# Kernel optimization log

Measured on AMD Instinct MI355X. Metric: run time of the kernel, lower is better.

Reference implementation:

```python
import jax, jax.numpy as jnp
import numpy as np

B, S, D = 4, 8192, 768
H, HD = 12, 64
CS, NL = 512, 32


def setup_inputs() -> dict:
    key = jax.random.key(0)
    ks = jax.random.split(key, 9)
    sc = 0.02
    return {
        "x": jax.random.normal(ks[0], (B, S, D), jnp.float32),
        "q_w": jax.random.normal(ks[1], (D, D), jnp.float32) * sc,
        "q_b": jax.random.normal(ks[2], (D,), jnp.float32) * sc,
        "k_w": jax.random.normal(ks[3], (D, D), jnp.float32) * sc,
        "k_b": jax.random.normal(ks[4], (D,), jnp.float32) * sc,
        "v_w": jax.random.normal(ks[5], (D, D), jnp.float32) * sc,
        "v_b": jax.random.normal(ks[6], (D,), jnp.float32) * sc,
        "o_w": jax.random.normal(ks[7], (D, D), jnp.float32) * sc,
        "o_b": jax.random.normal(ks[8], (D,), jnp.float32) * sc,
    }


def reference(x, q_w, q_b, k_w, k_b, v_w, v_b, o_w, o_b):
    # x: (B, S, D); S divisible by CS and NL -> no padding / trimming needed.
    scale = HD ** -0.5
    n_chunks = S // CS
    seg = S // NL
    # Global landmarks: mean-pool NL evenly spaced segments. (B, NL, D)
    landmarks = x.reshape(B, NL, seg, D).mean(axis=2)
    # Q only over local tokens (torch Linear: x @ W^T + b)
    q = (x @ q_w.T + q_b).reshape(B, n_chunks, CS, H, HD)
    x_chunks = x.reshape(B, n_chunks, CS, D)
    # Prepend landmarks to every chunk's KV context: ctx = NL + CS
    lm = jnp.broadcast_to(landmarks[:, None], (B, n_chunks, NL, D))
    kv_ctx = jnp.concatenate([lm, x_chunks], axis=2)  # (B, n_chunks, ctx, D)
    ctx = NL + CS
    k = (kv_ctx @ k_w.T + k_b).reshape(B, n_chunks, ctx, H, HD)
    v = (kv_ctx @ v_w.T + v_b).reshape(B, n_chunks, ctx, H, HD)
    scores = jnp.einsum("bnqhd,bnkhd->bnhqk", q, k) * scale
    attn = jax.nn.softmax(scores, axis=-1)  # dropout=0 (eval)
    out = jnp.einsum("bnhqk,bnkhd->bnqhd", attn, v).reshape(B, S, D)
    return out @ o_w.T + o_b
```

## Files before the change

kernel.cpp:

```cpp
#include <hip/hip_runtime.h>


typedef unsigned short u16;
typedef __attribute__((ext_vector_type(8))) short short8;
typedef __attribute__((ext_vector_type(4))) float f32x4;

__device__ __forceinline__ u16 f2bf(float f) {
    unsigned u = __float_as_uint(f);
    u += 0x7fffu + ((u >> 16) & 1u);
    return (u16)(u >> 16);
}

#define MFMA_BF16(A, B, C) __builtin_amdgcn_mfma_f32_16x16x32_bf16((A), (B), (C), 0, 0, 0)

__device__ __forceinline__ void gload16(const u16* g, const short* l) {
    __builtin_amdgcn_global_load_lds(
        (__attribute__((address_space(1))) void*)g,
        (__attribute__((address_space(3))) void*)l, 16, 0, 0);
}

__global__ __launch_bounds__(256) void k_cvtx(const float* __restrict__ x,
                                              u16* __restrict__ xa,
                                              float* __restrict__ part) {
    const int g = blockIdx.x;
    const int t = threadIdx.x;
    const float* base = x + (size_t)g * 64 * 768;
    u16* ob = xa + (size_t)g * 64 * 768;
    float s0 = 0.f, s1 = 0.f, s2 = 0.f;
    for (int r = 0; r < 64; ++r) {
        const size_t off = (size_t)r * 768;
        const float v0 = base[off + t], v1 = base[off + t + 256], v2 = base[off + t + 512];
        s0 += v0; s1 += v1; s2 += v2;
        ob[off + t] = f2bf(v0); ob[off + t + 256] = f2bf(v1); ob[off + t + 512] = f2bf(v2);
    }
    float* p = part + (size_t)g * 768;
    p[t] = s0; p[t + 256] = s1; p[t + 512] = s2;
}

__global__ void k_lmred(const float* __restrict__ part, u16* __restrict__ xa_lm) {
    const int bl = blockIdx.x;
    const int t = threadIdx.x;
    const float* p = part + (size_t)bl * 4 * 768;
    const float inv = 1.f / 256.f;
    for (int c = t; c < 768; c += 256) {
        const float s = p[c] + p[768 + c] + p[1536 + c] + p[2304 + c];
        xa_lm[(size_t)bl * 768 + c] = f2bf(s * inv);
    }
}

__global__ void k_cvtw(const float* __restrict__ qw, const float* __restrict__ kw,
                       const float* __restrict__ vw, const float* __restrict__ ow,
                       const float* __restrict__ qb, const float* __restrict__ kb,
                       const float* __restrict__ vb,
                       u16* __restrict__ wcat, u16* __restrict__ owb,
                       float* __restrict__ bcat) {
    const int yy = blockIdx.y;
    const int i = blockIdx.x * 256 + threadIdx.x;
    if (yy == 4) {
        if (i < 768)       bcat[i] = qb[i];
        else if (i < 1536) bcat[i] = kb[i - 768];
        else if (i < 2304) bcat[i] = vb[i - 1536];
        return;
    }
    const float* src = (yy == 0) ? qw : (yy == 1) ? kw : (yy == 2) ? vw : ow;
    u16* dst = (yy == 3) ? owb : wcat + (size_t)yy * 589824;
    const float4 v = ((const float4*)src)[i];
    ushort4 o;
    o.x = f2bf(v.x); o.y = f2bf(v.y); o.z = f2bf(v.z); o.w = f2bf(v.w);
    ((ushort4*)dst)[i] = o;
}

template <int MODE>
__global__ __launch_bounds__(512, 4) void k_gemm(
    const u16* __restrict__ A, const u16* __restrict__ Bw, const float* __restrict__ bias,
    u16* __restrict__ qx, u16* __restrict__ ktok, u16* __restrict__ vt,
    u16* __restrict__ klm, u16* __restrict__ vlmt, float* __restrict__ outf)
{
    __shared__ short lA[2][4096];
    __shared__ short lB[2][8192];
    const int t = threadIdx.x;
    const int wid = t >> 6, lane = t & 63, lr = lane & 15, lg = lane >> 4;
    const int wm = wid >> 2, wn = wid & 3;

    const int gx = gridDim.x;
    const int nwg = gx * gridDim.y;
    const int orig = blockIdx.x + gx * blockIdx.y;
    const int qq = nwg >> 3, rr = nwg & 7, xcd = orig & 7, ii = orig >> 3;
    const int wg = (xcd < rr ? xcd * (qq + 1) : rr * (qq + 1) + (xcd - rr) * qq) + ii;
    const int m0 = (wg / gx) * 128, n0 = (wg % gx) * 256;

    const int rA = t >> 2,        cA = ((t & 3) ^ ((rA >> 1) & 3)) * 8;
    const int rB0 = t >> 2,       cB0 = cA;
    const int uB1 = 512 + t;
    const int rB1 = uB1 >> 2,     cB1 = (((uB1) & 3) ^ ((rB1 >> 1) & 3)) * 8;
    const u16* pa0 = A  + (size_t)(m0 + rA) * 768 + cA;
    const u16* pb0 = Bw + (size_t)(n0 + rB0) * 768 + cB0;
    const u16* pb1 = Bw + (size_t)(n0 + rB1) * 768 + cB1;
    const int sa = (lg ^ ((lr >> 1) & 3)) * 8;

#define STG(S, T) {                                            \
    gload16(pa0 + (T) * 32, &lA[S][wid * 512]);                \
    gload16(pb0 + (T) * 32, &lB[S][wid * 512]);                \
    gload16(pb1 + (T) * 32, &lB[S][4096 + wid * 512]); }

    f32x4 acc[4][4] = {};
    STG(0, 0); STG(1, 1);

#pragma unroll
    for (int T = 0; T < 24; ++T) {
        const int s = T & 1;
        if (T < 23) asm volatile("s_waitcnt vmcnt(3)" ::: "memory");
        else        asm volatile("s_waitcnt vmcnt(0)" ::: "memory");
        __builtin_amdgcn_s_barrier();
        __builtin_amdgcn_sched_barrier(0);
        short8 aq[4], bq[4];
#pragma unroll
        for (int mf = 0; mf < 4; ++mf)
            aq[mf] = *(const short8*)&lA[s][(wm * 64 + mf * 16 + lr) * 32 + sa];
#pragma unroll
        for (int nf = 0; nf < 4; ++nf)
            bq[nf] = *(const short8*)&lB[s][(wn * 64 + nf * 16 + lr) * 32 + sa];
        asm volatile("s_waitcnt lgkmcnt(0)" ::: "memory");
        __builtin_amdgcn_sched_barrier(0);
        __builtin_amdgcn_s_barrier();
        if (T + 2 < 24) STG(s, T + 2);
        __builtin_amdgcn_s_setprio(1);
#pragma unroll
        for (int mf = 0; mf < 4; ++mf)
#pragma unroll
            for (int nf = 0; nf < 4; ++nf)
                acc[mf][nf] = MFMA_BF16(aq[mf], bq[nf], acc[mf][nf]);
        __builtin_amdgcn_s_setprio(0);
    }
#undef STG

    if (MODE == 0) {
        const int region = n0 / 768;
        if (region == 2) {
#pragma unroll
            for (int nf = 0; nf < 4; ++nf) {
                const int gn = n0 + wn * 64 + nf * 16 + lr;
                const float bv = bias[gn];
                const int nn = gn - 1536;
                const int h = nn >> 6, d = nn & 63;
#pragma unroll
                for (int mf = 0; mf < 4; ++mf) {
                    const int gmb = m0 + wm * 64 + mf * 16 + lg * 4;
                    ushort4 w;
                    w.x = f2bf(acc[mf][nf][0] + bv);
                    w.y = f2bf(acc[mf][nf][1] + bv);
                    w.z = f2bf(acc[mf][nf][2] + bv);
                    w.w = f2bf(acc[mf][nf][3] + bv);
                    if (gmb < 32768) {
                        const int b = gmb >> 13, ss = gmb & 8191;
                        *(ushort4*)(vt + ((size_t)(b * 12 + h) * 64 + d) * 8192 + ss) = w;
                    } else {
                        const int ii2 = gmb - 32768;
                        const int bb = ii2 >> 5, lmr = ii2 & 31;
                        *(ushort4*)(vlmt + ((size_t)(bb * 12 + h) * 64 + d) * 32 + lmr) = w;
                    }
                }
            }
        } else {
            u16* dst = (region == 0) ? qx : ktok;
#pragma unroll
            for (int nf = 0; nf < 4; ++nf) {
                const int gn = n0 + wn * 64 + nf * 16 + lr;
                const int nn = gn - region * 768;
                const int h = nn >> 6, d = nn & 63;
                const float bv = bias[gn];
#pragma unroll
                for (int mf = 0; mf < 4; ++mf) {
                    const int gmb = m0 + wm * 64 + mf * 16 + lg * 4;
#pragma unroll
                    for (int r = 0; r < 4; ++r) {
                        const int gm = gmb + r;
                        const u16 val = f2bf(acc[mf][nf][r] + bv);
                        if (gm < 32768) {
                            const int b = gm >> 13, ss = gm & 8191;
                            dst[((size_t)(b * 12 + h) * 8192 + ss) * 64 + d] = val;
                        } else if (region == 1) {
                            const int ii2 = gm - 32768;
                            klm[((size_t)((ii2 >> 5) * 12 + h) * 32 + (ii2 & 31)) * 64 + d] = val;
                        }
                    }
                }
            }
        }
    } else {
#pragma unroll
        for (int nf = 0; nf < 4; ++nf) {
            const int gn = n0 + wn * 64 + nf * 16 + lr;
            const float bvv = bias[gn];
#pragma unroll
            for (int mf = 0; mf < 4; ++mf) {
                const int gmb = m0 + wm * 64 + mf * 16 + lg * 4;
#pragma unroll
                for (int r = 0; r < 4; ++r)
                    outf[(size_t)(gmb + r) * 768 + gn] = acc[mf][nf][r] + bvv;
            }
        }
    }
}

__global__ __launch_bounds__(256) void k_attn(
    const u16* __restrict__ q, const u16* __restrict__ ktok,
    const u16* __restrict__ klm, const u16* __restrict__ vt,
    const u16* __restrict__ vlmt, u16* __restrict__ ao)
{
    __shared__ short kls[2][32 * 72];
    __shared__ short vls[2][64 * 40];
    __shared__ short pls[4][64 * 40];
    const int t = threadIdx.x, wid = t >> 6, l = t & 63, lr = l & 15, lg = l >> 4;
    const int idx = blockIdx.x;
    const int qt = idx & 1;
    const int h  = (idx >> 1) % 12;
    const int cb = (idx >> 1) / 12;
    const int c  = cb & 15, b = cb >> 4;
    const int bh = b * 12 + h;
    const int sb = c * 512 + qt * 256 + wid * 64;

    short8 qf[4][2];
#pragma unroll
    for (int mf = 0; mf < 4; ++mf)
#pragma unroll
        for (int kf = 0; kf < 2; ++kf)
            qf[mf][kf] = *(const short8*)(q + ((size_t)bh * 8192 + sb + mf * 16 + lr) * 64
                                            + kf * 32 + lg * 8);

    f32x4 O[4][4] = {};
    float lsum[4][4] = {};

    short* pw = &pls[wid][0];
    const int kn = t >> 3, kko = (t & 7) * 8;
    const int kctx = (kn < 16) ? (kn * 2) : ((kn - 16) * 2 + 1);
    const int vd = t >> 2, vco = (t & 3) * 8;

    auto kaddr = [&](int ti) -> const u16* {
        if (ti == 0) return klm + ((size_t)bh * 32 + kctx) * 64 + kko;
        return ktok + ((size_t)bh * 8192 + c * 512 + (ti - 1) * 32 + kctx) * 64 + kko;
    };
    auto vaddr = [&](int ti) -> const u16* {
        if (ti == 0) return vlmt + ((size_t)bh * 64 + vd) * 32 + vco;
        return vt + ((size_t)bh * 64 + vd) * 8192 + c * 512 + (ti - 1) * 32 + vco;
    };

    {
        const uint4 rk0 = *(const uint4*)kaddr(0);
        const uint4 rv0 = *(const uint4*)vaddr(0);
        *(uint4*)&kls[0][kn * 72 + kko] = rk0;
        *(uint4*)&vls[0][vd * 40 + vco] = rv0;
    }
    __syncthreads();

    for (int ti = 0; ti < 17; ++ti) {
        const int cur = ti & 1, nxt = cur ^ 1;
        uint4 rk, rv;
        if (ti < 16) { rk = *(const uint4*)kaddr(ti + 1); rv = *(const uint4*)vaddr(ti + 1); }

        f32x4 sc[4][2] = {};
#pragma unroll
        for (int kf = 0; kf < 2; ++kf) {
            const short8 b0 = *(const short8*)&kls[cur][(lr)      * 72 + kf * 32 + lg * 8];
            const short8 b1 = *(const short8*)&kls[cur][(16 + lr) * 72 + kf * 32 + lg * 8];
#pragma unroll
            for (int mf = 0; mf < 4; ++mf) {
                sc[mf][0] = MFMA_BF16(qf[mf][kf], b0, sc[mf][0]);
                sc[mf][1] = MFMA_BF16(qf[mf][kf], b1, sc[mf][1]);
            }
        }

#pragma unroll
        for (int mf = 0; mf < 4; ++mf) {
#pragma unroll
            for (int r = 0; r < 4; ++r) {
                const float p0 = __expf(sc[mf][0][r] * 0.125f);
                const float p1 = __expf(sc[mf][1][r] * 0.125f);
                lsum[mf][r] += p0 + p1;
                unsigned pk;
                asm("v_cvt_pk_bf16_f32 %0, %1, %2" : "=v"(pk) : "v"(p0), "v"(p1));
                const int prow = mf * 16 + lg * 4 + r;
                ((unsigned*)pw)[prow * 20 + lr] = pk;
            }
        }

        short8 vb[4];
#pragma unroll
        for (int df = 0; df < 4; ++df)
            vb[df] = *(const short8*)&vls[cur][(df * 16 + lr) * 40 + lg * 8];
#pragma unroll
        for (int mf = 0; mf < 4; ++mf) {
            const short8 pa2 = *(const short8*)&pw[(mf * 16 + lr) * 40 + lg * 8];
#pragma unroll
            for (int df = 0; df < 4; ++df)
                O[mf][df] = MFMA_BF16(pa2, vb[df], O[mf][df]);
        }

        if (ti < 16) {
            *(uint4*)&kls[nxt][kn * 72 + kko] = rk;
            *(uint4*)&vls[nxt][vd * 40 + vco] = rv;
        }
        __syncthreads();
    }

#pragma unroll
    for (int mf = 0; mf < 4; ++mf)
#pragma unroll
        for (int r = 0; r < 4; ++r) {
            float lv = lsum[mf][r];
            lv += __shfl_xor(lv, 1); lv += __shfl_xor(lv, 2);
            lv += __shfl_xor(lv, 4); lv += __shfl_xor(lv, 8);
            const float inv = 1.f / lv;
            const int srow = sb + mf * 16 + lg * 4 + r;
#pragma unroll
            for (int df = 0; df < 4; ++df)
                ao[((size_t)b * 8192 + srow) * 768 + h * 64 + df * 16 + lr] =
                    f2bf(O[mf][df][r] * inv);
        }
}

extern "C" void kernel_launch(void* const* d_in, const int* in_sizes, int n_in,
                              void* d_out, int out_size, void* d_ws, size_t ws_size,
                              hipStream_t stream)
{
    const float* x  = (const float*)d_in[0];
    const float* qw = (const float*)d_in[1];
    const float* qb = (const float*)d_in[2];
    const float* kw = (const float*)d_in[3];
    const float* kb = (const float*)d_in[4];
    const float* vw = (const float*)d_in[5];
    const float* vb = (const float*)d_in[6];
    const float* ow = (const float*)d_in[7];
    const float* ob = (const float*)d_in[8];
    float* out = (float*)d_out;

    u16* xa     = (u16*)d_ws;
    u16* wcat   = xa + (size_t)32896 * 768;
    u16* owb    = wcat + (size_t)2304 * 768;
    float* bcat = (float*)(owb + (size_t)768 * 768);
    u16* qx     = (u16*)(bcat + 2304);
    u16* ktok   = qx   + (size_t)32768 * 768;
    u16* vt     = ktok + (size_t)32768 * 768;
    u16* klm    = vt + (size_t)32768 * 768;
    u16* vlmt   = klm + 98304;
    float* part = (float*)(vlmt + 98304);
    u16* ao     = xa;

    k_cvtx<<<512, 256, 0, stream>>>(x, xa, part);
    k_lmred<<<128, 256, 0, stream>>>(part, xa + (size_t)32768 * 768);
    k_cvtw<<<dim3(576, 5), 256, 0, stream>>>(qw, kw, vw, ow, qb, kb, vb, wcat, owb, bcat);

    k_gemm<0><<<dim3(9, 257), 512, 0, stream>>>(xa, wcat, bcat,
                                                qx, ktok, vt, klm, vlmt, nullptr);
    k_attn<<<1536, 256, 0, stream>>>(qx, ktok, klm, vt, vlmt, ao);
    k_gemm<1><<<dim3(3, 256), 512, 0, stream>>>(ao, owb, ob,
                                                nullptr, nullptr, nullptr, nullptr, nullptr, out);
}
```

Before: 351.6 us.

## Triple-buffer GEMM LDS stages and vectorize x conversion with finer partial sums

After: 365.2 us. 1.04x slower.

```diff
diff --git a/kernel.cpp b/kernel.cpp
--- a/kernel.cpp
+++ b/kernel.cpp
@@ -21,29 +21,41 @@
 
 __global__ __launch_bounds__(256) void k_cvtx(const float* __restrict__ x,
                                               u16* __restrict__ xa,
-                                              float* __restrict__ part) {
+                                              float* __restrict__ part2) {
     const int g = blockIdx.x;
-    const int t = threadIdx.x;
+    const int t = threadIdx.x, q = t >> 6, l = t & 63;
     const float* base = x + (size_t)g * 64 * 768;
     u16* ob = xa + (size_t)g * 64 * 768;
-    float s0 = 0.f, s1 = 0.f, s2 = 0.f;
-    for (int r = 0; r < 64; ++r) {
-        const size_t off = (size_t)r * 768;
-        const float v0 = base[off + t], v1 = base[off + t + 256], v2 = base[off + t + 512];
-        s0 += v0; s1 += v1; s2 += v2;
-        ob[off + t] = f2bf(v0); ob[off + t + 256] = f2bf(v1); ob[off + t + 512] = f2bf(v2);
-    }
-    float* p = part + (size_t)g * 768;
-    p[t] = s0; p[t + 256] = s1; p[t + 512] = s2;
-}
-
-__global__ void k_lmred(const float* __restrict__ part, u16* __restrict__ xa_lm) {
+    float s[3][4] = {};
+    for (int it = 0; it < 16; ++it) {
+        const size_t ro = (size_t)(it * 4 + q) * 768;
+#pragma unroll
+        for (int k = 0; k < 3; ++k) {
+            const int c4 = (l + k * 64) * 4;
+            const float4 v = *(const float4*)(base + ro + c4);
+            s[k][0] += v.x; s[k][1] += v.y; s[k][2] += v.z; s[k][3] += v.w;
+            ushort4 o;
+            o.x = f2bf(v.x); o.y = f2bf(v.y); o.z = f2bf(v.z); o.w = f2bf(v.w);
+            *(ushort4*)(ob + ro + c4) = o;
+        }
+    }
+    float* p = part2 + (size_t)(g * 4 + q) * 768;
+#pragma unroll
+    for (int k = 0; k < 3; ++k)
+#pragma unroll
+        for (int j = 0; j < 4; ++j)
+            p[(l + k * 64) * 4 + j] = s[k][j];
+}
+
+__global__ void k_lmred(const float* __restrict__ part2, u16* __restrict__ xa_lm) {
     const int bl = blockIdx.x;
     const int t = threadIdx.x;
-    const float* p = part + (size_t)bl * 4 * 768;
+    const float* p = part2 + (size_t)bl * 16 * 768;
     const float inv = 1.f / 256.f;
     for (int c = t; c < 768; c += 256) {
-        const float s = p[c] + p[768 + c] + p[1536 + c] + p[2304 + c];
+        float s = 0.f;
+#pragma unroll
+        for (int i = 0; i < 16; ++i) s += p[i * 768 + c];
         xa_lm[(size_t)bl * 768 + c] = f2bf(s * inv);
     }
 }
@@ -76,8 +88,8 @@
     u16* __restrict__ qx, u16* __restrict__ ktok, u16* __restrict__ vt,
     u16* __restrict__ klm, u16* __restrict__ vlmt, float* __restrict__ outf)
 {
-    __shared__ short lA[2][4096];
-    __shared__ short lB[2][8192];
+    __shared__ short lA[3][4096];
+    __shared__ short lB[3][8192];
     const int t = threadIdx.x;
     const int wid = t >> 6, lane = t & 63, lr = lane & 15, lg = lane >> 4;
     const int wm = wid >> 2, wn = wid & 3;
@@ -89,12 +101,11 @@
     const int wg = (xcd < rr ? xcd * (qq + 1) : rr * (qq + 1) + (xcd - rr) * qq) + ii;
     const int m0 = (wg / gx) * 128, n0 = (wg % gx) * 256;
 
-    const int rA = t >> 2,        cA = ((t & 3) ^ ((rA >> 1) & 3)) * 8;
-    const int rB0 = t >> 2,       cB0 = cA;
+    const int rA = t >> 2,  cA = ((t & 3) ^ ((rA >> 1) & 3)) * 8;
     const int uB1 = 512 + t;
-    const int rB1 = uB1 >> 2,     cB1 = (((uB1) & 3) ^ ((rB1 >> 1) & 3)) * 8;
+    const int rB1 = uB1 >> 2, cB1 = ((uB1 & 3) ^ ((rB1 >> 1) & 3)) * 8;
     const u16* pa0 = A  + (size_t)(m0 + rA) * 768 + cA;
-    const u16* pb0 = Bw + (size_t)(n0 + rB0) * 768 + cB0;
+    const u16* pb0 = Bw + (size_t)(n0 + rA) * 768 + cA;
     const u16* pb1 = Bw + (size_t)(n0 + rB1) * 768 + cB1;
     const int sa = (lg ^ ((lr >> 1) & 3)) * 8;
 
@@ -108,11 +119,11 @@
 
 #pragma unroll
     for (int T = 0; T < 24; ++T) {
-        const int s = T & 1;
+        const int s = T % 3;
         if (T < 23) asm volatile("s_waitcnt vmcnt(3)" ::: "memory");
         else        asm volatile("s_waitcnt vmcnt(0)" ::: "memory");
         __builtin_amdgcn_s_barrier();
-        __builtin_amdgcn_sched_barrier(0);
+        if (T + 2 < 24) STG((T + 2) % 3, T + 2);
         short8 aq[4], bq[4];
 #pragma unroll
         for (int mf = 0; mf < 4; ++mf)
@@ -120,10 +131,6 @@
 #pragma unroll
         for (int nf = 0; nf < 4; ++nf)
             bq[nf] = *(const short8*)&lB[s][(wn * 64 + nf * 16 + lr) * 32 + sa];
-        asm volatile("s_waitcnt lgkmcnt(0)" ::: "memory");
-        __builtin_amdgcn_sched_barrier(0);
-        __builtin_amdgcn_s_barrier();
-        if (T + 2 < 24) STG(s, T + 2);
         __builtin_amdgcn_s_setprio(1);
 #pragma unroll
         for (int mf = 0; mf < 4; ++mf)
@@ -343,11 +350,11 @@
     u16* vt     = ktok + (size_t)32768 * 768;
     u16* klm    = vt + (size_t)32768 * 768;
     u16* vlmt   = klm + 98304;
-    float* part = (float*)(vlmt + 98304);
+    float* part2= (float*)(vlmt + 98304);
     u16* ao     = xa;
 
-    k_cvtx<<<512, 256, 0, stream>>>(x, xa, part);
-    k_lmred<<<128, 256, 0, stream>>>(part, xa + (size_t)32768 * 768);
+    k_cvtx<<<512, 256, 0, stream>>>(x, xa, part2);
+    k_lmred<<<128, 256, 0, stream>>>(part2, xa + (size_t)32768 * 768);
     k_cvtw<<<dim3(576, 5), 256, 0, stream>>>(qw, kw, vw, ow, qb, kb, vb, wcat, owb, bcat);
 
     k_gemm<0><<<dim3(9, 257), 512, 0, stream>>>(xa, wcat, bcat,
```
